# Optimization experiments

Hardware: AMD Instinct MI355X
Metric: run time of the kernel (lower is better)

The kernel has to match this reference:

```python
import jax, jax.numpy as jnp
import numpy as np

B, S, IN, H = 256, 512, 512, 512

def setup_inputs() -> dict:
    key = jax.random.key(0)
    ks = jax.random.split(key, 8)
    s = 1.0 / np.sqrt(H)
    si = 1.0 / np.sqrt(IN)
    return {
        "inputs": jax.random.normal(ks[0], (B, S, IN), dtype=jnp.float32),
        "timestamps": jax.random.uniform(ks[1], (B, S), dtype=jnp.float32),
        "W_all_w": jax.random.uniform(ks[2], (4 * H, H), dtype=jnp.float32, minval=-s, maxval=s),
        "W_all_b": jax.random.uniform(ks[3], (4 * H,), dtype=jnp.float32, minval=-s, maxval=s),
        "U_all_w": jax.random.uniform(ks[4], (4 * H, IN), dtype=jnp.float32, minval=-si, maxval=si),
        "U_all_b": jax.random.uniform(ks[5], (4 * H,), dtype=jnp.float32, minval=-si, maxval=si),
        "W_d_w": jax.random.uniform(ks[6], (H, H), dtype=jnp.float32, minval=-s, maxval=s),
        "W_d_b": jax.random.uniform(ks[7], (H,), dtype=jnp.float32, minval=-s, maxval=s),
    }

def reference(inputs, timestamps, W_all_w, W_all_b, U_all_w, U_all_b, W_d_w, W_d_b):
    b, seq, _ = inputs.shape
    hsz = W_d_w.shape[0]
    # Precompute input projections for all steps at once: [B,S,4H]
    u_proj = jnp.einsum('bsi,gi->bsg', inputs, U_all_w) + U_all_b

    def step(carry, xs):
        h, c = carry
        u_t, t_t = xs  # u_t: [B,4H], t_t: [B]
        c_s1 = jnp.tanh(c @ W_d_w.T + W_d_b)
        c_adj = c - c_s1 + c_s1 * t_t[:, None]
        outs = h @ W_all_w.T + W_all_b + u_t
        f, i, o, c_tmp = jnp.split(outs, 4, axis=1)
        f = jax.nn.sigmoid(f)
        i = jax.nn.sigmoid(i)
        o = jax.nn.sigmoid(o)
        c_tmp = jnp.tanh(c_tmp)
        c = f * c_adj + i * c_tmp
        h = o * jnp.tanh(c)
        return (h, c), (o, h, c)

    h0 = jnp.zeros((b, hsz), dtype=inputs.dtype)
    c0 = jnp.zeros((b, hsz), dtype=inputs.dtype)
    (h, c), (o_seq, h_seq, c_seq) = jax.lax.scan(
        step, (h0, c0),
        (jnp.swapaxes(u_proj, 0, 1), jnp.swapaxes(timestamps, 0, 1)))
    outputs = jnp.swapaxes(o_seq, 0, 1)  # [B,S,H]
    return outputs, h, c
```

## Files before the change

kernel.cpp:

```cpp
#include <hip/hip_runtime.h>
#include <hip/hip_bf16.h>
#include <math.h>

#define BATCH 256
#define SEQ   512
#define IN_D  512
#define HID   512
#define FOURH 2048
#define BS_ROWS (BATCH * SEQ)

typedef __bf16 bf16x8 __attribute__((ext_vector_type(8)));
typedef float  f32x4  __attribute__((ext_vector_type(4)));
typedef unsigned uint32x4 __attribute__((ext_vector_type(4)));
typedef unsigned long long ull;

__device__ __forceinline__ float sigf(float x)  { return 1.0f / (1.0f + __expf(-x)); }
__device__ __forceinline__ float tanhf_(float x){ return 1.0f - 2.0f / (__expf(2.0f * x) + 1.0f); }

__global__ __launch_bounds__(256) void init_kernel(
    const float* __restrict__ W_all_w, const float* __restrict__ W_all_b,
    const float* __restrict__ U_all_w, const float* __restrict__ U_all_b,
    const float* __restrict__ W_d_w,
    __bf16* __restrict__ Wb, __bf16* __restrict__ Ub, __bf16* __restrict__ Db,
    float* __restrict__ bias_all,
    unsigned* __restrict__ hc,
    unsigned* __restrict__ bar)
{
    const int stride = gridDim.x * blockDim.x;
    const int tid0 = blockIdx.x * blockDim.x + threadIdx.x;

    const int nW = FOURH * HID;
    for (int i = tid0; i < nW; i += stride) {
        Wb[i] = (__bf16)W_all_w[i];
        Ub[i] = (__bf16)U_all_w[i];
    }
    const int nD = HID * HID;
    for (int i = tid0; i < nD; i += stride) Db[i] = (__bf16)W_d_w[i];
    for (int i = tid0; i < FOURH; i += stride) bias_all[i] = W_all_b[i] + U_all_b[i];
    for (int i = tid0; i < 2 * BATCH * HID; i += stride) hc[i] = 0u;
    for (int i = tid0; i < 16 * 2 * 32; i += stride) bar[i] = 0u;
}

__global__ __launch_bounds__(256) void uproj_gemm(
    const float* __restrict__ x, const __bf16* __restrict__ Ub,
    __bf16* __restrict__ up)
{
    const unsigned bid = blockIdx.x;
    const unsigned lg = (bid & 7) * 2048u + (bid >> 3);
    const int cb = lg & 15;
    const int rb = lg >> 4;

    __shared__ __bf16 As[128][64];
    __shared__ __bf16 Bs[128][64];

    const int tid = threadIdx.x;
    const int wave = tid >> 6, lane = tid & 63;
    const int wm = wave >> 1, wn = wave & 1;
    const int lrow = lane & 15, kq = lane >> 4;
    const int sw = (lrow & 7) << 3;

    f32x4 acc[4][4];
    #pragma unroll
    for (int m = 0; m < 4; ++m)
        #pragma unroll
        for (int n = 0; n < 4; ++n) acc[m][n] = (f32x4){0.f, 0.f, 0.f, 0.f};

    const int srow = tid >> 1;
    const int skc  = (tid & 1) * 32;
    const int dsw  = (srow & 7) << 3;

    for (int kk = 0; kk < 512; kk += 64) {
        {
            const float* xs = x + (size_t)(rb * 128 + srow) * 512 + kk + skc;
            #pragma unroll
            for (int j = 0; j < 4; ++j) {
                float4 va = ((const float4*)xs)[2 * j];
                float4 vb = ((const float4*)xs)[2 * j + 1];
                bf16x8 pk;
                pk[0] = (__bf16)va.x; pk[1] = (__bf16)va.y;
                pk[2] = (__bf16)va.z; pk[3] = (__bf16)va.w;
                pk[4] = (__bf16)vb.x; pk[5] = (__bf16)vb.y;
                pk[6] = (__bf16)vb.z; pk[7] = (__bf16)vb.w;
                *(bf16x8*)&As[srow][(skc + j * 8) ^ dsw] = pk;
            }
            const __bf16* bsrc = Ub + (size_t)(cb * 128 + srow) * 512 + kk + skc;
            #pragma unroll
            for (int j = 0; j < 4; ++j)
                *(uint4*)&Bs[srow][(skc + j * 8) ^ dsw] = *(const uint4*)(bsrc + j * 8);
        }
        __syncthreads();

        #pragma unroll
        for (int k2 = 0; k2 < 2; ++k2) {
            const int ke = k2 * 32 + kq * 8;
            bf16x8 af[4], bfr[4];
            #pragma unroll
            for (int m = 0; m < 4; ++m)
                af[m] = *(const bf16x8*)&As[wm * 64 + m * 16 + lrow][ke ^ sw];
            #pragma unroll
            for (int n = 0; n < 4; ++n)
                bfr[n] = *(const bf16x8*)&Bs[wn * 64 + n * 16 + lrow][ke ^ sw];
            #pragma unroll
            for (int m = 0; m < 4; ++m)
                #pragma unroll
                for (int n = 0; n < 4; ++n)
                    acc[m][n] = __builtin_amdgcn_mfma_f32_16x16x32_bf16(af[m], bfr[n], acc[m][n], 0, 0, 0);
        }
        __syncthreads();
    }

    const int colL = lane & 15, r0 = (lane >> 4) * 4;
    const size_t orow0 = (size_t)rb * 128 + wm * 64;
    const int ocol0 = cb * 128 + wn * 64;
    #pragma unroll
    for (int m = 0; m < 4; ++m)
        #pragma unroll
        for (int n = 0; n < 4; ++n)
            #pragma unroll
            for (int i = 0; i < 4; ++i)
                up[(orow0 + m * 16 + r0 + i) * 2048 + ocol0 + n * 16 + colL] = (__bf16)acc[m][n][i];
}

__global__ __launch_bounds__(512) void scan_kernel(
    const __bf16* __restrict__ up,
    const float* __restrict__ timestamps,
    const __bf16* __restrict__ Wb,
    const __bf16* __restrict__ Db,
    const float* __restrict__ bias_all,
    const float* __restrict__ Wd_b,
    unsigned* __restrict__ hc,
    unsigned* __restrict__ bar,
    float* __restrict__ out)
{
    const int tid = threadIdx.x;
    const int bid = blockIdx.x;
    const int grp = bid & 15, blk = bid >> 4;
    const int b0 = grp * 16;
    const int k0 = blk * 32;
    const int wave = tid >> 6, lane = tid & 63;
    const int ct = wave >> 2, kq4 = wave & 3;
    const int lrow = lane & 15, kq = lane >> 4;
    const int swz = (lrow & 7) << 3;
    const int k0w = k0 + ct * 16;
    const int kbase = kq4 * 128 + kq * 8;

    __shared__ __bf16 Ah[16][512];
    __shared__ __bf16 Ac[16][512];
    __shared__ float  exg[8][4][16][19];
    __shared__ float  exd[2][4][16][19];
    __shared__ __bf16 Us[2][16][128];
    __shared__ float  Ts[2][16];
    __shared__ float  Cm[512];
    __shared__ float  BiasW[128];
    __shared__ float  BiasD[32];

    bf16x8 Bg[4][4], Bd4[4];
    #pragma unroll
    for (int u = 0; u < 4; ++u)
        #pragma unroll
        for (int ks = 0; ks < 4; ++ks)
            Bg[u][ks] = *(const bf16x8*)(Wb + (size_t)(u * 512 + k0w + lrow) * 512 + kbase + ks * 32);
    #pragma unroll
    for (int ks = 0; ks < 4; ++ks)
        Bd4[ks] = *(const bf16x8*)(Db + (size_t)(k0w + lrow) * 512 + kbase + ks * 32);

    if (tid < 128) BiasW[tid] = bias_all[(tid >> 5) * 512 + k0 + (tid & 31)];
    else if (tid < 160) BiasD[tid - 128] = Wd_b[k0 + (tid - 128)];
    Cm[tid] = 0.f;
    if (tid < 256) {
        const int row = tid >> 4, j = tid & 15, g = j >> 2, seg = j & 3;
        uint32x4 v = __builtin_nontemporal_load(
            (const uint32x4*)(up + ((size_t)(b0 + row) * 512 + 0) * 2048
                              + g * 512 + k0 + seg * 8));
        *(uint32x4*)&Us[0][row][g * 32 + seg * 8] = v;
    }
    if (tid < 16) Ts[0][tid] = timestamps[(size_t)(b0 + tid) * 512 + 0];
    __syncthreads();

    #pragma unroll 1
    for (int t = 0; t < SEQ; ++t) {
        const int par = t & 1;

        if (t > 0) {
            if (tid < 16) {
                unsigned* fl = &bar[(grp * 2 + par) * 32 + tid];
                while (__hip_atomic_load(fl, __ATOMIC_RELAXED,
                                         __HIP_MEMORY_SCOPE_AGENT) < (unsigned)t)
                    __builtin_amdgcn_s_sleep(1);
            }
            __syncthreads();
        }

        {
            const ull* src = (const ull*)(hc + (size_t)par * BATCH * HID) + (size_t)b0 * 256;
            ull v[8];
            #pragma unroll
            for (int i = 0; i < 8; ++i)
                v[i] = __hip_atomic_load(src + i * 512 + tid, __ATOMIC_RELAXED,
                                         __HIP_MEMORY_SCOPE_AGENT);
            #pragma unroll
            for (int i = 0; i < 8; ++i) {
                const int m = i * 512 + tid;
                const int row = m >> 8;
                const int cp = (m & 255) * 2;
                const unsigned lo = (unsigned)v[i];
                const unsigned hi = (unsigned)(v[i] >> 32);
                const unsigned h2 = (lo & 0xFFFFu) | (hi << 16);
                const unsigned c2 = (lo >> 16) | (hi & 0xFFFF0000u);
                const int d = cp ^ ((row & 7) << 3);
                *(unsigned*)&Ah[row][d] = h2;
                *(unsigned*)&Ac[row][d] = c2;
            }
        }
        __syncthreads();

        uint32x4 upf;
        float tpf = 0.f;
        const bool do_pf = (t + 1 < SEQ);
        if (do_pf && tid < 256) {
            const int row = tid >> 4, j = tid & 15, g = j >> 2, seg = j & 3;
            upf = __builtin_nontemporal_load(
                (const uint32x4*)(up + ((size_t)(b0 + row) * 512 + (t + 1)) * 2048
                                  + g * 512 + k0 + seg * 8));
        }
        if (do_pf && tid < 16) tpf = timestamps[(size_t)(b0 + tid) * 512 + (t + 1)];

        f32x4 ag[4], ad;
        #pragma unroll
        for (int u = 0; u < 4; ++u) ag[u] = (f32x4){0.f, 0.f, 0.f, 0.f};
        ad = (f32x4){0.f, 0.f, 0.f, 0.f};
        #pragma unroll
        for (int ks = 0; ks < 4; ++ks) {
            const int koff = (kbase + ks * 32) ^ swz;
            bf16x8 a_h = *(const bf16x8*)&Ah[lrow][koff];
            #pragma unroll
            for (int u = 0; u < 4; ++u)
                ag[u] = __builtin_amdgcn_mfma_f32_16x16x32_bf16(a_h, Bg[u][ks], ag[u], 0, 0, 0);
            bf16x8 a_c = *(const bf16x8*)&Ac[lrow][koff];
            ad = __builtin_amdgcn_mfma_f32_16x16x32_bf16(a_c, Bd4[ks], ad, 0, 0, 0);
        }

        if (do_pf && tid < 256) {
            const int row = tid >> 4, j = tid & 15, g = j >> 2, seg = j & 3;
            *(uint32x4*)&Us[par ^ 1][row][g * 32 + seg * 8] = upf;
        }
        if (do_pf && tid < 16) Ts[par ^ 1][tid] = tpf;

        {
            const int colL = lane & 15, r0 = kq * 4;
            #pragma unroll
            for (int u = 0; u < 4; ++u)
                #pragma unroll
                for (int i = 0; i < 4; ++i)
                    exg[u * 2 + ct][kq4][r0 + i][colL] = ag[u][i];
            #pragma unroll
            for (int i = 0; i < 4; ++i)
                exd[ct][kq4][r0 + i][colL] = ad[i];
        }
        __syncthreads();

        float o_def = 0.f;
        {
            const int r = tid >> 5, kcol = tid & 31;
            const int ctg = kcol >> 4, k16 = kcol & 15;
            float g4[4];
            #pragma unroll
            for (int g = 0; g < 4; ++g)
                g4[g] = BiasW[g * 32 + kcol] + (float)Us[par][r][g * 32 + kcol]
                      + exg[g * 2 + ctg][0][r][k16] + exg[g * 2 + ctg][1][r][k16]
                      + exg[g * 2 + ctg][2][r][k16] + exg[g * 2 + ctg][3][r][k16];
            float dd = BiasD[kcol]
                     + exd[ctg][0][r][k16] + exd[ctg][1][r][k16]
                     + exd[ctg][2][r][k16] + exd[ctg][3][r][k16];

            const float c_old = Cm[tid];
            const float tt = Ts[par][r];
            const float c_s1  = tanhf_(dd);
            const float c_adj = c_old - c_s1 + c_s1 * tt;
            const float f  = sigf(g4[0]);
            const float ii = sigf(g4[1]);
            const float o  = sigf(g4[2]);
            const float c_tmp = tanhf_(g4[3]);
            const float c_new = f * c_adj + ii * c_tmp;
            const float h_new = o * tanhf_(c_new);
            Cm[tid] = c_new;

            if (t == SEQ - 1) {
                __builtin_nontemporal_store(o,
                    &out[((size_t)(b0 + r) * 512 + t) * 512 + k0 + kcol]);
                const size_t base = (size_t)BATCH * SEQ * HID;
                out[base + (size_t)(b0 + r) * 512 + k0 + kcol] = h_new;
                out[base + (size_t)BATCH * HID + (size_t)(b0 + r) * 512 + k0 + kcol] = c_new;
            } else {
                o_def = o;
                const unsigned hb16 = (unsigned)__builtin_bit_cast(unsigned short, (__bf16)h_new);
                const unsigned cb16 = (unsigned)__builtin_bit_cast(unsigned short, (__bf16)c_new);
                const unsigned pk = hb16 | (cb16 << 16);
                unsigned* dst = hc + (size_t)(par ^ 1) * BATCH * HID
                                   + (size_t)(b0 + r) * 512 + k0 + kcol;
                __hip_atomic_store(dst, pk, __ATOMIC_RELAXED, __HIP_MEMORY_SCOPE_AGENT);
            }
        }
        __syncthreads();

        if (t < SEQ - 1) {
            if (tid == 0)
                __hip_atomic_store(&bar[(grp * 2 + ((t + 1) & 1)) * 32 + blk],
                                   (unsigned)(t + 1),
                                   __ATOMIC_RELAXED, __HIP_MEMORY_SCOPE_AGENT);
            {
                const int r = tid >> 5, kcol = tid & 31;
                __builtin_nontemporal_store(o_def,
                    &out[((size_t)(b0 + r) * 512 + t) * 512 + k0 + kcol]);
            }
        }
    }
}

extern "C" void kernel_launch(void* const* d_in, const int* in_sizes, int n_in,
                              void* d_out, int out_size, void* d_ws, size_t ws_size,
                              hipStream_t stream) {
    const float* inputs     = (const float*)d_in[0];
    const float* timestamps = (const float*)d_in[1];
    const float* W_all_w    = (const float*)d_in[2];
    const float* W_all_b    = (const float*)d_in[3];
    const float* U_all_w    = (const float*)d_in[4];
    const float* U_all_b    = (const float*)d_in[5];
    const float* W_d_w      = (const float*)d_in[6];
    const float* W_d_b      = (const float*)d_in[7];
    float* out = (float*)d_out;

    char* ws = (char*)d_ws;
    size_t off = 0;
    auto alloc = [&](size_t bytes) -> void* {
        void* p = ws + off;
        off += (bytes + 255) & ~(size_t)255;
        return p;
    };
    __bf16* Wb       = (__bf16*)alloc((size_t)FOURH * HID * 2);
    __bf16* Ub       = (__bf16*)alloc((size_t)FOURH * HID * 2);
    __bf16* Db       = (__bf16*)alloc((size_t)HID * HID * 2);
    float*  bias_all = (float*) alloc((size_t)FOURH * 4);
    unsigned* hcbuf  = (unsigned*)alloc((size_t)2 * BATCH * HID * 4);
    unsigned* bar    = (unsigned*)alloc(16 * 2 * 32 * 4);
    __bf16* up       = (__bf16*)alloc((size_t)BS_ROWS * FOURH * 2);

    hipLaunchKernelGGL(init_kernel, dim3(1024), dim3(256), 0, stream,
                       W_all_w, W_all_b, U_all_w, U_all_b, W_d_w,
                       Wb, Ub, Db, bias_all, hcbuf, bar);

    hipLaunchKernelGGL(uproj_gemm, dim3(16384), dim3(256), 0, stream,
                       inputs, Ub, up);

    void* sargs[] = {
        (void*)&up, (void*)&timestamps, (void*)&Wb, (void*)&Db,
        (void*)&bias_all, (void*)&W_d_b,
        (void*)&hcbuf, (void*)&bar, (void*)&out
    };
    hipLaunchCooperativeKernel((const void*)scan_kernel, dim3(256), dim3(512),
                               sargs, 0, stream);
}
```

Measured before the change: 2.277 ms.

## Specialize scan waves into gate and decay roles with per-wave flag polling

```diff
diff --git a/kernel.cpp b/kernel.cpp
--- a/kernel.cpp
+++ b/kernel.cpp
@@ -23,7 +23,8 @@
     const float* __restrict__ W_d_w,
     __bf16* __restrict__ Wb, __bf16* __restrict__ Ub, __bf16* __restrict__ Db,
     float* __restrict__ bias_all,
-    unsigned* __restrict__ hc,
+    unsigned* __restrict__ hb,
+    unsigned* __restrict__ cb,
     unsigned* __restrict__ bar)
 {
     const int stride = gridDim.x * blockDim.x;
@@ -37,7 +38,7 @@
     const int nD = HID * HID;
     for (int i = tid0; i < nD; i += stride) Db[i] = (__bf16)W_d_w[i];
     for (int i = tid0; i < FOURH; i += stride) bias_all[i] = W_all_b[i] + U_all_b[i];
-    for (int i = tid0; i < 2 * BATCH * HID; i += stride) hc[i] = 0u;
+    for (int i = tid0; i < 2 * BATCH * 256; i += stride) { hb[i] = 0u; cb[i] = 0u; }
     for (int i = tid0; i < 16 * 2 * 32; i += stride) bar[i] = 0u;
 }
 
@@ -121,14 +122,15 @@
                 up[(orow0 + m * 16 + r0 + i) * 2048 + ocol0 + n * 16 + colL] = (__bf16)acc[m][n][i];
 }
 
-__global__ __launch_bounds__(512) void scan_kernel(
+__global__ __launch_bounds__(512, 2) void scan_kernel(
     const __bf16* __restrict__ up,
     const float* __restrict__ timestamps,
     const __bf16* __restrict__ Wb,
     const __bf16* __restrict__ Db,
     const float* __restrict__ bias_all,
     const float* __restrict__ Wd_b,
-    unsigned* __restrict__ hc,
+    unsigned* __restrict__ hbuf,
+    unsigned* __restrict__ cbuf,
     unsigned* __restrict__ bar,
     float* __restrict__ out)
 {
@@ -138,31 +140,41 @@
     const int b0 = grp * 16;
     const int k0 = blk * 32;
     const int wave = tid >> 6, lane = tid & 63;
-    const int ct = wave >> 2, kq4 = wave & 3;
+    const int wq = wave & 3;
+    const bool is_d = (wave >= 4);
     const int lrow = lane & 15, kq = lane >> 4;
     const int swz = (lrow & 7) << 3;
-    const int k0w = k0 + ct * 16;
-    const int kbase = kq4 * 128 + kq * 8;
+    const int kbase = wq * 128 + kq * 8;
 
     __shared__ __bf16 Ah[16][512];
     __shared__ __bf16 Ac[16][512];
-    __shared__ float  exg[8][4][16][19];
-    __shared__ float  exd[2][4][16][19];
+    __shared__ float  exg[4][16][33][4];
+    __shared__ float  exd[16][33][4];
     __shared__ __bf16 Us[2][16][128];
     __shared__ float  Ts[2][16];
     __shared__ float  Cm[512];
     __shared__ float  BiasW[128];
     __shared__ float  BiasD[32];
 
-    bf16x8 Bg[4][4], Bd4[4];
-    #pragma unroll
-    for (int u = 0; u < 4; ++u)
-        #pragma unroll
-        for (int ks = 0; ks < 4; ++ks)
-            Bg[u][ks] = *(const bf16x8*)(Wb + (size_t)(u * 512 + k0w + lrow) * 512 + kbase + ks * 32);
-    #pragma unroll
-    for (int ks = 0; ks < 4; ++ks)
-        Bd4[ks] = *(const bf16x8*)(Db + (size_t)(k0w + lrow) * 512 + kbase + ks * 32);
+    bf16x8 Bg[4][2][4];
+    bf16x8 Bd[2][4];
+    if (!is_d) {
+        #pragma unroll
+        for (int u = 0; u < 4; ++u)
+            #pragma unroll
+            for (int ct = 0; ct < 2; ++ct)
+                #pragma unroll
+                for (int ks = 0; ks < 4; ++ks)
+                    Bg[u][ct][ks] = *(const bf16x8*)(
+                        Wb + (size_t)(u * 512 + k0 + ct * 16 + lrow) * 512 + kbase + ks * 32);
+    } else {
+        #pragma unroll
+        for (int ct = 0; ct < 2; ++ct)
+            #pragma unroll
+            for (int ks = 0; ks < 4; ++ks)
+                Bd[ct][ks] = *(const bf16x8*)(
+                    Db + (size_t)(k0 + ct * 16 + lrow) * 512 + kbase + ks * 32);
+    }
 
     if (tid < 128) BiasW[tid] = bias_all[(tid >> 5) * 512 + k0 + (tid & 31)];
     else if (tid < 160) BiasD[tid - 128] = Wd_b[k0 + (tid - 128)];
@@ -182,96 +194,110 @@
         const int par = t & 1;
 
         if (t > 0) {
-            if (tid < 16) {
-                unsigned* fl = &bar[(grp * 2 + par) * 32 + tid];
-                while (__hip_atomic_load(fl, __ATOMIC_RELAXED,
-                                         __HIP_MEMORY_SCOPE_AGENT) < (unsigned)t)
-                    __builtin_amdgcn_s_sleep(1);
-            }
-            __syncthreads();
+            const unsigned* fl = &bar[(grp * 2 + par) * 32 + wq * 4];
+            for (;;) {
+                unsigned f = (lane < 4)
+                    ? __hip_atomic_load(&fl[lane], __ATOMIC_RELAXED, __HIP_MEMORY_SCOPE_AGENT)
+                    : 0xFFFFFFFFu;
+                if (__all((int)(f >= (unsigned)t))) break;
+                __builtin_amdgcn_s_sleep(1);
+            }
         }
 
         {
-            const ull* src = (const ull*)(hc + (size_t)par * BATCH * HID) + (size_t)b0 * 256;
+            const ull* src = (const ull*)(is_d ? cbuf : hbuf)
+                           + (size_t)par * 32768 + (size_t)b0 * 128 + wq * 32 + (lane & 31);
             ull v[8];
             #pragma unroll
-            for (int i = 0; i < 8; ++i)
-                v[i] = __hip_atomic_load(src + i * 512 + tid, __ATOMIC_RELAXED,
-                                         __HIP_MEMORY_SCOPE_AGENT);
-            #pragma unroll
-            for (int i = 0; i < 8; ++i) {
-                const int m = i * 512 + tid;
-                const int row = m >> 8;
-                const int cp = (m & 255) * 2;
-                const unsigned lo = (unsigned)v[i];
-                const unsigned hi = (unsigned)(v[i] >> 32);
-                const unsigned h2 = (lo & 0xFFFFu) | (hi << 16);
-                const unsigned c2 = (lo >> 16) | (hi & 0xFFFF0000u);
-                const int d = cp ^ ((row & 7) << 3);
-                *(unsigned*)&Ah[row][d] = h2;
-                *(unsigned*)&Ac[row][d] = c2;
-            }
-        }
-        __syncthreads();
-
-        uint32x4 upf;
-        float tpf = 0.f;
+            for (int l = 0; l < 8; ++l)
+                v[l] = __hip_atomic_load(src + (size_t)(2 * l + (lane >> 5)) * 128,
+                                         __ATOMIC_RELAXED, __HIP_MEMORY_SCOPE_AGENT);
+            __bf16 (* __restrict__ dst)[512] = is_d ? Ac : Ah;
+            #pragma unroll
+            for (int l = 0; l < 8; ++l) {
+                const int row = 2 * l + (lane >> 5);
+                const int e = (wq * 128 + (lane & 31) * 4) ^ ((row & 7) << 3);
+                *(ull*)&dst[row][e] = v[l];
+            }
+        }
+        asm volatile("s_waitcnt lgkmcnt(0)" ::: "memory");
+        __builtin_amdgcn_sched_barrier(0);
+
         const bool do_pf = (t + 1 < SEQ);
-        if (do_pf && tid < 256) {
-            const int row = tid >> 4, j = tid & 15, g = j >> 2, seg = j & 3;
-            upf = __builtin_nontemporal_load(
-                (const uint32x4*)(up + ((size_t)(b0 + row) * 512 + (t + 1)) * 2048
-                                  + g * 512 + k0 + seg * 8));
-        }
-        if (do_pf && tid < 16) tpf = timestamps[(size_t)(b0 + tid) * 512 + (t + 1)];
-
-        f32x4 ag[4], ad;
-        #pragma unroll
-        for (int u = 0; u < 4; ++u) ag[u] = (f32x4){0.f, 0.f, 0.f, 0.f};
-        ad = (f32x4){0.f, 0.f, 0.f, 0.f};
-        #pragma unroll
-        for (int ks = 0; ks < 4; ++ks) {
-            const int koff = (kbase + ks * 32) ^ swz;
-            bf16x8 a_h = *(const bf16x8*)&Ah[lrow][koff];
+        if (!is_d) {
+            f32x4 acc[4][2];
             #pragma unroll
             for (int u = 0; u < 4; ++u)
-                ag[u] = __builtin_amdgcn_mfma_f32_16x16x32_bf16(a_h, Bg[u][ks], ag[u], 0, 0, 0);
-            bf16x8 a_c = *(const bf16x8*)&Ac[lrow][koff];
-            ad = __builtin_amdgcn_mfma_f32_16x16x32_bf16(a_c, Bd4[ks], ad, 0, 0, 0);
-        }
-
-        if (do_pf && tid < 256) {
-            const int row = tid >> 4, j = tid & 15, g = j >> 2, seg = j & 3;
-            *(uint32x4*)&Us[par ^ 1][row][g * 32 + seg * 8] = upf;
-        }
-        if (do_pf && tid < 16) Ts[par ^ 1][tid] = tpf;
-
-        {
-            const int colL = lane & 15, r0 = kq * 4;
+                #pragma unroll
+                for (int ct = 0; ct < 2; ++ct) acc[u][ct] = (f32x4){0.f, 0.f, 0.f, 0.f};
+            #pragma unroll
+            for (int ks = 0; ks < 4; ++ks) {
+                bf16x8 a = *(const bf16x8*)&Ah[lrow][(kbase + ks * 32) ^ swz];
+                #pragma unroll
+                for (int u = 0; u < 4; ++u)
+                    #pragma unroll
+                    for (int ct = 0; ct < 2; ++ct)
+                        acc[u][ct] = __builtin_amdgcn_mfma_f32_16x16x32_bf16(
+                            a, Bg[u][ct][ks], acc[u][ct], 0, 0, 0);
+            }
+            const int colL = lane & 15;
             #pragma unroll
             for (int u = 0; u < 4; ++u)
                 #pragma unroll
+                for (int ct = 0; ct < 2; ++ct)
+                    #pragma unroll
+                    for (int i = 0; i < 4; ++i)
+                        exg[u][kq * 4 + i][ct * 16 + colL][wq] = acc[u][ct][i];
+        } else {
+            uint32x4 upf;
+            float tpf = 0.f;
+            const int tid2 = tid - 256;
+            if (do_pf) {
+                const int row = tid2 >> 4, j = tid2 & 15, g = j >> 2, seg = j & 3;
+                upf = __builtin_nontemporal_load(
+                    (const uint32x4*)(up + ((size_t)(b0 + row) * 512 + (t + 1)) * 2048
+                                      + g * 512 + k0 + seg * 8));
+                if (tid2 < 16) tpf = timestamps[(size_t)(b0 + tid2) * 512 + (t + 1)];
+            }
+
+            f32x4 accd[2];
+            accd[0] = (f32x4){0.f, 0.f, 0.f, 0.f};
+            accd[1] = (f32x4){0.f, 0.f, 0.f, 0.f};
+            #pragma unroll
+            for (int ks = 0; ks < 4; ++ks) {
+                bf16x8 a = *(const bf16x8*)&Ac[lrow][(kbase + ks * 32) ^ swz];
+                #pragma unroll
+                for (int ct = 0; ct < 2; ++ct)
+                    accd[ct] = __builtin_amdgcn_mfma_f32_16x16x32_bf16(
+                        a, Bd[ct][ks], accd[ct], 0, 0, 0);
+            }
+            const int colL = lane & 15;
+            #pragma unroll
+            for (int ct = 0; ct < 2; ++ct)
+                #pragma unroll
                 for (int i = 0; i < 4; ++i)
-                    exg[u * 2 + ct][kq4][r0 + i][colL] = ag[u][i];
-            #pragma unroll
-            for (int i = 0; i < 4; ++i)
-                exd[ct][kq4][r0 + i][colL] = ad[i];
+                    exd[kq * 4 + i][ct * 16 + colL][wq] = accd[ct][i];
+
+            if (do_pf) {
+                const int row = tid2 >> 4, j = tid2 & 15, g = j >> 2, seg = j & 3;
+                *(uint32x4*)&Us[par ^ 1][row][g * 32 + seg * 8] = upf;
+                if (tid2 < 16) Ts[par ^ 1][tid2] = tpf;
+            }
         }
         __syncthreads();
 
         float o_def = 0.f;
         {
             const int r = tid >> 5, kcol = tid & 31;
-            const int ctg = kcol >> 4, k16 = kcol & 15;
+            f32x4 pd = *(const f32x4*)&exd[r][kcol][0];
             float g4[4];
             #pragma unroll
-            for (int g = 0; g < 4; ++g)
+            for (int g = 0; g < 4; ++g) {
+                f32x4 p = *(const f32x4*)&exg[g][r][kcol][0];
                 g4[g] = BiasW[g * 32 + kcol] + (float)Us[par][r][g * 32 + kcol]
-                      + exg[g * 2 + ctg][0][r][k16] + exg[g * 2 + ctg][1][r][k16]
-                      + exg[g * 2 + ctg][2][r][k16] + exg[g * 2 + ctg][3][r][k16];
-            float dd = BiasD[kcol]
-                     + exd[ctg][0][r][k16] + exd[ctg][1][r][k16]
-                     + exd[ctg][2][r][k16] + exd[ctg][3][r][k16];
+                      + (p[0] + p[1]) + (p[2] + p[3]);
+            }
+            const float dd = BiasD[kcol] + (pd[0] + pd[1]) + (pd[2] + pd[3]);
 
             const float c_old = Cm[tid];
             const float tt = Ts[par][r];
@@ -295,10 +321,16 @@
                 o_def = o;
                 const unsigned hb16 = (unsigned)__builtin_bit_cast(unsigned short, (__bf16)h_new);
                 const unsigned cb16 = (unsigned)__builtin_bit_cast(unsigned short, (__bf16)c_new);
-                const unsigned pk = hb16 | (cb16 << 16);
-                unsigned* dst = hc + (size_t)(par ^ 1) * BATCH * HID
-                                   + (size_t)(b0 + r) * 512 + k0 + kcol;
-                __hip_atomic_store(dst, pk, __ATOMIC_RELAXED, __HIP_MEMORY_SCOPE_AGENT);
+                const unsigned hn = (unsigned)__shfl_xor((int)hb16, 1);
+                const unsigned cn = (unsigned)__shfl_xor((int)cb16, 1);
+                if (!(lane & 1)) {
+                    const unsigned hp = hb16 | (hn << 16);
+                    const unsigned cp = cb16 | (cn << 16);
+                    const size_t e = (size_t)(par ^ 1) * 65536
+                                   + (size_t)(b0 + r) * 256 + ((k0 + kcol) >> 1);
+                    __hip_atomic_store(hbuf + e, hp, __ATOMIC_RELAXED, __HIP_MEMORY_SCOPE_AGENT);
+                    __hip_atomic_store(cbuf + e, cp, __ATOMIC_RELAXED, __HIP_MEMORY_SCOPE_AGENT);
+                }
             }
         }
         __syncthreads();
@@ -341,13 +373,14 @@
     __bf16* Ub       = (__bf16*)alloc((size_t)FOURH * HID * 2);
     __bf16* Db       = (__bf16*)alloc((size_t)HID * HID * 2);
     float*  bias_all = (float*) alloc((size_t)FOURH * 4);
-    unsigned* hcbuf  = (unsigned*)alloc((size_t)2 * BATCH * HID * 4);
+    unsigned* hbuf   = (unsigned*)alloc((size_t)2 * BATCH * 256 * 4);
+    unsigned* cbuf   = (unsigned*)alloc((size_t)2 * BATCH * 256 * 4);
     unsigned* bar    = (unsigned*)alloc(16 * 2 * 32 * 4);
     __bf16* up       = (__bf16*)alloc((size_t)BS_ROWS * FOURH * 2);
 
     hipLaunchKernelGGL(init_kernel, dim3(1024), dim3(256), 0, stream,
                        W_all_w, W_all_b, U_all_w, U_all_b, W_d_w,
-                       Wb, Ub, Db, bias_all, hcbuf, bar);
+                       Wb, Ub, Db, bias_all, hbuf, cbuf, bar);
 
     hipLaunchKernelGGL(uproj_gemm, dim3(16384), dim3(256), 0, stream,
                        inputs, Ub, up);
@@ -355,7 +388,7 @@
     void* sargs[] = {
         (void*)&up, (void*)&timestamps, (void*)&Wb, (void*)&Db,
         (void*)&bias_all, (void*)&W_d_b,
-        (void*)&hcbuf, (void*)&bar, (void*)&out
+        (void*)&hbuf, (void*)&cbuf, (void*)&bar, (void*)&out
     };
     hipLaunchCooperativeKernel((const void*)scan_kernel, dim3(256), dim3(512),
                                sargs, 0, stream);
```

Result: slower. 2.471 ms (+8.5%).
